# Kernel optimization log

Hardware: AMD Instinct MI355X
Metric: run time of the kernel (lower is better)

The kernel has to match this reference:

```python
import jax, jax.numpy as jnp
import numpy as np

B, N, DH = 256, 32, 128      # batch, n_agents, per-agent hidden
E = 496                       # n_edges (fully connected over 32 agents)
DIM_IN = 2 * DH               # 256, MLP input (concat of two agent states)
DIM_HID = 256
A = 12                        # dim_act
R = 4                         # payoff_rank
DIM_OUT = 2 * R * A           # 96


def setup_inputs() -> dict:
    key = jax.random.key(0)
    ks = jax.random.split(key, 7)
    hidden_states_n = jax.random.normal(ks[0], (B, N, DH), dtype=jnp.float32)
    edges_from = jax.random.randint(ks[1], (E,), 0, N, dtype=jnp.int32).astype(jnp.int64)
    edges_to = jax.random.randint(ks[2], (E,), 0, N, dtype=jnp.int32).astype(jnp.int64)
    # torch.nn.Linear params: W [out, in], b [out]
    W1 = jax.random.normal(ks[3], (DIM_HID, DIM_IN), dtype=jnp.float32) * (1.0 / np.sqrt(DIM_IN))
    b1 = jnp.zeros((DIM_HID,), dtype=jnp.float32)
    W2 = jax.random.normal(ks[4], (DIM_OUT, DIM_HID), dtype=jnp.float32) * (1.0 / np.sqrt(DIM_HID))
    b2 = jnp.zeros((DIM_OUT,), dtype=jnp.float32)
    return {"hidden_states_n": hidden_states_n, "W1": W1, "b1": b1, "W2": W2,
            "b2": b2, "edges_from": edges_from, "edges_to": edges_to}


def reference(hidden_states_n, W1, b1, W2, b2, edges_from, edges_to):
    hf = hidden_states_n[:, edges_from]                     # [B, E, DH]
    ht = hidden_states_n[:, edges_to]                       # [B, E, DH]
    # stack of (from||to, to||from): [2, B, E, 2*DH]
    inp = jnp.stack([jnp.concatenate([hf, ht], axis=-1),
                     jnp.concatenate([ht, hf], axis=-1)], axis=0)
    h = jax.nn.relu(inp @ W1.T + b1)                        # [2, B, E, DIM_HID]
    p = h @ W2.T + b2                                       # [2, B, E, 2*R*A]
    p = p.reshape(2, B, E, R, 2, A)
    # low-rank outer product per rank, summed over ranks: [2, B, E, A, A]
    payoffs = jnp.einsum('sberi,sberj->sbeij', p[..., 0, :], p[..., 1, :])
    # second copy is transposed, then mean over the two directions
    return 0.5 * (payoffs[0] + jnp.swapaxes(payoffs[1], -1, -2))  # [B, E, A, A]
```

## Files before the change

kernel.cpp:

```cpp
#include <hip/hip_runtime.h>

typedef unsigned int uint;
typedef unsigned short ushort_t;
typedef _Float16 f16;

typedef __attribute__((ext_vector_type(8))) _Float16 f16x8;
typedef __attribute__((ext_vector_type(2))) _Float16 f16x2;
typedef __attribute__((ext_vector_type(4))) float f32x4;

#define E_CNT 496

__device__ __forceinline__ uint pack2_f16(float lo, float hi) {
    union { f16x2 h; uint u; } r;
    r.h[0] = (_Float16)lo;
    r.h[1] = (_Float16)hi;
    return r.u;
}

__global__ __launch_bounds__(256) void x_kernel(
    const float* __restrict__ hidden, const float* __restrict__ W1,
    const float* __restrict__ b1, f16* __restrict__ Xout) {
    __shared__ __align__(16) f16 w1s[256 * 128];

    const int tid = threadIdx.x;
    const int half = blockIdx.x & 1;
    const int mblk = blockIdx.x >> 1;

    {
        const int c = tid & 15;
        const int h0 = tid >> 4;
        #pragma unroll
        for (int it = 0; it < 16; ++it) {
            const int h = it * 16 + h0;
            const float* src = W1 + h * 256 + half * 128 + c * 8;
            float4 v0 = *(const float4*)src;
            float4 v1 = *(const float4*)(src + 4);
            uint4 o;
            o.x = pack2_f16(v0.x, v0.y);
            o.y = pack2_f16(v0.z, v0.w);
            o.z = pack2_f16(v1.x, v1.y);
            o.w = pack2_f16(v1.z, v1.w);
            *(uint4*)&w1s[h * 128 + ((c ^ (h & 7)) << 3)] = o;
        }
    }

    const int ln = tid & 63;
    const int waveId = tid >> 6;
    const int quad = ln >> 4;
    const int l16 = ln & 15;
    const int row0 = mblk * 64 + waveId * 16;

    union { uint u[4]; f16x8 v; } af[4];
    const float* arow = hidden + (row0 + l16) * 128 + quad * 8;
    #pragma unroll
    for (int kk = 0; kk < 4; ++kk) {
        float4 v0 = *(const float4*)(arow + kk * 32);
        float4 v1 = *(const float4*)(arow + kk * 32 + 4);
        af[kk].u[0] = pack2_f16(v0.x, v0.y);
        af[kk].u[1] = pack2_f16(v0.z, v0.w);
        af[kk].u[2] = pack2_f16(v1.x, v1.y);
        af[kk].u[3] = pack2_f16(v1.z, v1.w);
    }
    float bh[16];
    #pragma unroll
    for (int nt = 0; nt < 16; ++nt) bh[nt] = 0.5f * b1[nt * 16 + l16];

    __syncthreads();

    f16* xbase = Xout + half * (8192 * 256);
    #pragma unroll 4
    for (int nt = 0; nt < 16; ++nt) {
        const int h = nt * 16 + l16;
        f32x4 acc = (f32x4){0.f, 0.f, 0.f, 0.f};
        #pragma unroll
        for (int kk = 0; kk < 4; ++kk) {
            const int c_log = kk * 4 + quad;
            f16x8 bf = *(const f16x8*)&w1s[h * 128 + ((c_log ^ (h & 7)) << 3)];
            acc = __builtin_amdgcn_mfma_f32_16x16x32_f16(af[kk].v, bf, acc, 0, 0, 0);
        }
        #pragma unroll
        for (int r = 0; r < 4; ++r) {
            const int row = row0 + quad * 4 + r;
            xbase[row * 256 + h] = (_Float16)(acc[r] + bh[nt]);
        }
    }
}

#define PAIR_STRIDE 100
#define R_OFF 800
#define WAVE_PF 1600

__global__ __launch_bounds__(512, 4) void gemm_payoff_kernel(
    const f16* __restrict__ X1, const f16* __restrict__ X2,
    const int* __restrict__ e_f, const int* __restrict__ e_t,
    const float* __restrict__ W2, const float* __restrict__ b2,
    float* __restrict__ out) {

    __shared__ __align__(16) unsigned char smem[51200];
    f16* w2s = (f16*)smem;
    float* pf = (float*)smem;

    const int tid = threadIdx.x;

    #pragma unroll
    for (int j = 0; j < 12; ++j) {
        int idx4 = tid + j * 512;
        int n = idx4 >> 6;
        int k = (idx4 & 63) << 2;
        float4 v = *(const float4*)&W2[n * 256 + k];
        uint2 o;
        o.x = pack2_f16(v.x, v.y);
        o.y = pack2_f16(v.z, v.w);
        *(uint2*)&w2s[n * 264 + k] = o;
    }

    const int ln = tid & 63;
    const int waveId = tid >> 6;
    const int quad = ln >> 4;
    const int l16 = ln & 15;
    const int pl = l16 & 7;
    const int s = l16 >> 3;

    const int bx = blockIdx.x;
    const int lb = (bx & 7) * 124 + (bx >> 3);

    bool f64 = true, t64 = true;
    #pragma unroll
    for (int i = 0; i < 16; ++i) {
        if (e_f[2 * i + 1] != 0) f64 = false;
        if (e_t[2 * i + 1] != 0) t64 = false;
    }

    const int pairBase = lb * 128 + waveId * 16;
    const f16* px1[2];
    const f16* px2[2];
    #pragma unroll
    for (int mt = 0; mt < 2; ++mt) {
        int pair = pairBase + mt * 8 + pl;
        int b = pair / E_CNT;
        int e = pair - b * E_CNT;
        int f = f64 ? e_f[2 * e] : e_f[e];
        int t = t64 ? e_t[2 * e] : e_t[e];
        int n1 = s ? t : f;
        int n2 = s ? f : t;
        px1[mt] = X1 + ((b * 32 + n1) * 256 + quad * 8);
        px2[mt] = X2 + ((b * 32 + n2) * 256 + quad * 8);
    }

    f32x4 acc[2][6];
    #pragma unroll
    for (int mt = 0; mt < 2; ++mt)
        #pragma unroll
        for (int tt = 0; tt < 6; ++tt) acc[mt][tt] = (f32x4){0.f, 0.f, 0.f, 0.f};

    typedef union { uint4 q; f16x8 h; } XU;
    XU G1[2][2], G2[2][2];

    #pragma unroll
    for (int mt = 0; mt < 2; ++mt) {
        G1[0][mt].q = *(const uint4*)(px1[mt] + 0 * 32);
        G2[0][mt].q = *(const uint4*)(px2[mt] + 0 * 32);
        G1[1][mt].q = *(const uint4*)(px1[mt] + 1 * 32);
        G2[1][mt].q = *(const uint4*)(px2[mt] + 1 * 32);
    }

    const f16x8 zero8 = (f16x8){0, 0, 0, 0, 0, 0, 0, 0};

    __syncthreads();

    #pragma unroll
    for (int kk = 0; kk < 8; ++kk) {
        const int buf = kk & 1;
        f16x8 af[2];
        #pragma unroll
        for (int mt = 0; mt < 2; ++mt) {
            f16x8 sum = G1[buf][mt].h + G2[buf][mt].h;
            af[mt] = __builtin_elementwise_max(sum, zero8);
        }
        if (kk < 6) {
            #pragma unroll
            for (int mt = 0; mt < 2; ++mt) {
                G1[buf][mt].q = *(const uint4*)(px1[mt] + (kk + 2) * 32);
                G2[buf][mt].q = *(const uint4*)(px2[mt] + (kk + 2) * 32);
            }
        }
        #pragma unroll
        for (int tt = 0; tt < 6; ++tt) {
            f16x8 bf = *(const f16x8*)&w2s[(tt * 16 + l16) * 264 + kk * 32 + quad * 8];
            acc[0][tt] = __builtin_amdgcn_mfma_f32_16x16x32_f16(af[0], bf, acc[0][tt], 0, 0, 0);
            acc[1][tt] = __builtin_amdgcn_mfma_f32_16x16x32_f16(af[1], bf, acc[1][tt], 0, 0, 0);
        }
    }

    float b2v[6];
    #pragma unroll
    for (int tt = 0; tt < 6; ++tt) b2v[tt] = b2[tt * 16 + l16];

    __syncthreads();

    float* wbase = pf + waveId * WAVE_PF;
    #pragma unroll
    for (int mt = 0; mt < 2; ++mt) {
        #pragma unroll
        for (int tt = 0; tt < 6; ++tt) {
            const int n = tt * 16 + l16;
            const int rr = n / 24;
            const int rem = n - rr * 24;
            const int c01 = (rem >= 12) ? 1 : 0;
            const int a = rem - c01 * 12;
            #pragma unroll
            for (int r = 0; r < 4; ++r) {
                const int row = quad * 4 + r;
                const int s_ = row >> 3;
                const int pl_ = row & 7;
                const int k8 = (s_ ? 4 : 0) + rr;
                const int toL = (c01 == s_) ? 1 : 0;
                wbase[(toL ? 0 : R_OFF) + pl_ * PAIR_STRIDE + a * 8 + k8] = acc[mt][tt][r] + b2v[tt];
            }
        }

        #pragma unroll
        for (int it = 0; it < 2; ++it) {
            int task = it * 64 + ln;
            if (task < 96) {
                int pp = task / 12;
                int i = task - pp * 12;
                const float* Lp = wbase + pp * PAIR_STRIDE + i * 8;
                float4 l0 = *(const float4*)&Lp[0];
                float4 l1 = *(const float4*)&Lp[4];
                float od[12];
                #pragma unroll
                for (int jj = 0; jj < 12; ++jj) {
                    const float* Rp = wbase + R_OFF + pp * PAIR_STRIDE + jj * 8;
                    float4 r0 = *(const float4*)&Rp[0];
                    float4 r1 = *(const float4*)&Rp[4];
                    float d = l0.x * r0.x + l0.y * r0.y + l0.z * r0.z + l0.w * r0.w
                            + l1.x * r1.x + l1.y * r1.y + l1.z * r1.z + l1.w * r1.w;
                    od[jj] = 0.5f * d;
                }
                int outBase = (pairBase + mt * 8 + pp) * 144 + i * 12;
                *(float4*)&out[outBase + 0] = make_float4(od[0], od[1], od[2], od[3]);
                *(float4*)&out[outBase + 4] = make_float4(od[4], od[5], od[6], od[7]);
                *(float4*)&out[outBase + 8] = make_float4(od[8], od[9], od[10], od[11]);
            }
        }
    }
}

extern "C" void kernel_launch(void* const* d_in, const int* in_sizes, int n_in,
                              void* d_out, int out_size, void* d_ws, size_t ws_size,
                              hipStream_t stream) {
    const float* hidden = (const float*)d_in[0];
    const float* W1 = (const float*)d_in[1];
    const float* b1 = (const float*)d_in[2];
    const float* W2 = (const float*)d_in[3];
    const float* b2 = (const float*)d_in[4];
    const int* e_f = (const int*)d_in[5];
    const int* e_t = (const int*)d_in[6];
    float* out = (float*)d_out;

    char* ws = (char*)d_ws;
    f16* X = (f16*)ws;

    x_kernel<<<256, 256, 0, stream>>>(hidden, W1, b1, X);
    gemm_payoff_kernel<<<992, 512, 0, stream>>>(X, X + 8192 * 256, e_f, e_t, W2, b2, out);
}
```

Measured before the change: 137.6 us.

## Restructure X kernel to keep W1 in registers; halve payoff blocks with split W2 staging

The first kernel now keeps each wave's W1 tiles in registers and stages a 64-row tile of hidden states in shared memory instead of staging a full f16 W1 half. It swaps the MFMA operands so each lane writes four packed f16 outputs at once, and it launches twice as many blocks. The payoff kernel drops to 256 threads per block and 26KB of shared memory by staging W2 in two K-halves with extra barriers, which should allow more resident blocks. Scatter offsets are also precomputed. The cost is reloading and converting W2 twice per block and more block-level synchronization.

```diff
diff --git a/kernel.cpp b/kernel.cpp
--- a/kernel.cpp
+++ b/kernel.cpp
@@ -1,7 +1,6 @@
 #include <hip/hip_runtime.h>
 
 typedef unsigned int uint;
-typedef unsigned short ushort_t;
 typedef _Float16 f16;
 
 typedef __attribute__((ext_vector_type(8))) _Float16 f16x8;
@@ -20,68 +19,81 @@
 __global__ __launch_bounds__(256) void x_kernel(
     const float* __restrict__ hidden, const float* __restrict__ W1,
     const float* __restrict__ b1, f16* __restrict__ Xout) {
-    __shared__ __align__(16) f16 w1s[256 * 128];
+    __shared__ __align__(16) float hs[64 * 132];
 
     const int tid = threadIdx.x;
-    const int half = blockIdx.x & 1;
-    const int mblk = blockIdx.x >> 1;
-
-    {
-        const int c = tid & 15;
-        const int h0 = tid >> 4;
-        #pragma unroll
-        for (int it = 0; it < 16; ++it) {
-            const int h = it * 16 + h0;
-            const float* src = W1 + h * 256 + half * 128 + c * 8;
-            float4 v0 = *(const float4*)src;
-            float4 v1 = *(const float4*)(src + 4);
-            uint4 o;
-            o.x = pack2_f16(v0.x, v0.y);
-            o.y = pack2_f16(v0.z, v0.w);
-            o.z = pack2_f16(v1.x, v1.y);
-            o.w = pack2_f16(v1.z, v1.w);
-            *(uint4*)&w1s[h * 128 + ((c ^ (h & 7)) << 3)] = o;
-        }
-    }
-
+    const int rowblock = blockIdx.x >> 2;
+    const int g = blockIdx.x & 3;
     const int ln = tid & 63;
     const int waveId = tid >> 6;
     const int quad = ln >> 4;
     const int l16 = ln & 15;
-    const int row0 = mblk * 64 + waveId * 16;
-
-    union { uint u[4]; f16x8 v; } af[4];
-    const float* arow = hidden + (row0 + l16) * 128 + quad * 8;
-    #pragma unroll
-    for (int kk = 0; kk < 4; ++kk) {
-        float4 v0 = *(const float4*)(arow + kk * 32);
-        float4 v1 = *(const float4*)(arow + kk * 32 + 4);
-        af[kk].u[0] = pack2_f16(v0.x, v0.y);
-        af[kk].u[1] = pack2_f16(v0.z, v0.w);
-        af[kk].u[2] = pack2_f16(v1.x, v1.y);
-        af[kk].u[3] = pack2_f16(v1.z, v1.w);
-    }
-    float bh[16];
-    #pragma unroll
-    for (int nt = 0; nt < 16; ++nt) bh[nt] = 0.5f * b1[nt * 16 + l16];
-
-    __syncthreads();
-
-    f16* xbase = Xout + half * (8192 * 256);
-    #pragma unroll 4
-    for (int nt = 0; nt < 16; ++nt) {
-        const int h = nt * 16 + l16;
-        f32x4 acc = (f32x4){0.f, 0.f, 0.f, 0.f};
+    const int row0 = rowblock * 64;
+
+    union FU { uint u[4]; f16x8 v; };
+    FU wf[2][4];
+    float bh[2][4];
+    #pragma unroll
+    for (int nt = 0; nt < 2; ++nt) {
+        const int t = (g * 4 + waveId) * 2 + nt;
+        const int half = t >> 4;
+        const int htile = t & 15;
+        const float* wrow = W1 + (htile * 16 + l16) * 256 + half * 128 + quad * 8;
         #pragma unroll
         for (int kk = 0; kk < 4; ++kk) {
-            const int c_log = kk * 4 + quad;
-            f16x8 bf = *(const f16x8*)&w1s[h * 128 + ((c_log ^ (h & 7)) << 3)];
-            acc = __builtin_amdgcn_mfma_f32_16x16x32_f16(af[kk].v, bf, acc, 0, 0, 0);
-        }
-        #pragma unroll
-        for (int r = 0; r < 4; ++r) {
-            const int row = row0 + quad * 4 + r;
-            xbase[row * 256 + h] = (_Float16)(acc[r] + bh[nt]);
+            float4 v0 = *(const float4*)(wrow + kk * 32);
+            float4 v1 = *(const float4*)(wrow + kk * 32 + 4);
+            wf[nt][kk].u[0] = pack2_f16(v0.x, v0.y);
+            wf[nt][kk].u[1] = pack2_f16(v0.z, v0.w);
+            wf[nt][kk].u[2] = pack2_f16(v1.x, v1.y);
+            wf[nt][kk].u[3] = pack2_f16(v1.z, v1.w);
+        }
+        #pragma unroll
+        for (int r = 0; r < 4; ++r)
+            bh[nt][r] = 0.5f * b1[htile * 16 + quad * 4 + r];
+    }
+
+    {
+        const float* src = hidden + row0 * 128;
+        #pragma unroll
+        for (int it = 0; it < 8; ++it) {
+            int idx = it * 256 + tid;
+            int r = idx >> 5;
+            int c4 = idx & 31;
+            float4 v = *(const float4*)(src + idx * 4);
+            *(float4*)&hs[r * 132 + c4 * 4] = v;
+        }
+    }
+    __syncthreads();
+
+    #pragma unroll
+    for (int ch = 0; ch < 4; ++ch) {
+        FU hf[4];
+        const float* hrow = &hs[(ch * 16 + l16) * 132 + quad * 8];
+        #pragma unroll
+        for (int kk = 0; kk < 4; ++kk) {
+            float4 v0 = *(const float4*)(hrow + kk * 32);
+            float4 v1 = *(const float4*)(hrow + kk * 32 + 4);
+            hf[kk].u[0] = pack2_f16(v0.x, v0.y);
+            hf[kk].u[1] = pack2_f16(v0.z, v0.w);
+            hf[kk].u[2] = pack2_f16(v1.x, v1.y);
+            hf[kk].u[3] = pack2_f16(v1.z, v1.w);
+        }
+        #pragma unroll
+        for (int nt = 0; nt < 2; ++nt) {
+            const int t = (g * 4 + waveId) * 2 + nt;
+            const int half = t >> 4;
+            const int htile = t & 15;
+            f32x4 acc = (f32x4){0.f, 0.f, 0.f, 0.f};
+            #pragma unroll
+            for (int kk = 0; kk < 4; ++kk)
+                acc = __builtin_amdgcn_mfma_f32_16x16x32_f16(wf[nt][kk].v, hf[kk].v, acc, 0, 0, 0);
+            uint2 o;
+            o.x = pack2_f16(acc[0] + bh[nt][0], acc[1] + bh[nt][1]);
+            o.y = pack2_f16(acc[2] + bh[nt][2], acc[3] + bh[nt][3]);
+            f16* dst = Xout + half * (8192 * 256)
+                     + (row0 + ch * 16 + l16) * 256 + htile * 16 + quad * 4;
+            *(uint2*)dst = o;
         }
     }
 }
@@ -90,30 +102,17 @@
 #define R_OFF 800
 #define WAVE_PF 1600
 
-__global__ __launch_bounds__(512, 4) void gemm_payoff_kernel(
+__global__ __launch_bounds__(256, 4) void gemm_payoff_kernel(
     const f16* __restrict__ X1, const f16* __restrict__ X2,
     const int* __restrict__ e_f, const int* __restrict__ e_t,
     const float* __restrict__ W2, const float* __restrict__ b2,
     float* __restrict__ out) {
 
-    __shared__ __align__(16) unsigned char smem[51200];
+    __shared__ __align__(16) unsigned char smem[26624];
     f16* w2s = (f16*)smem;
     float* pf = (float*)smem;
 
     const int tid = threadIdx.x;
-
-    #pragma unroll
-    for (int j = 0; j < 12; ++j) {
-        int idx4 = tid + j * 512;
-        int n = idx4 >> 6;
-        int k = (idx4 & 63) << 2;
-        float4 v = *(const float4*)&W2[n * 256 + k];
-        uint2 o;
-        o.x = pack2_f16(v.x, v.y);
-        o.y = pack2_f16(v.z, v.w);
-        *(uint2*)&w2s[n * 264 + k] = o;
-    }
-
     const int ln = tid & 63;
     const int waveId = tid >> 6;
     const int quad = ln >> 4;
@@ -122,7 +121,7 @@
     const int s = l16 >> 3;
 
     const int bx = blockIdx.x;
-    const int lb = (bx & 7) * 124 + (bx >> 3);
+    const int lb = (bx & 7) * 248 + (bx >> 3);
 
     bool f64 = true, t64 = true;
     #pragma unroll
@@ -131,7 +130,7 @@
         if (e_t[2 * i + 1] != 0) t64 = false;
     }
 
-    const int pairBase = lb * 128 + waveId * 16;
+    const int pairBase = lb * 64 + waveId * 16;
     const f16* px1[2];
     const f16* px2[2];
     #pragma unroll
@@ -164,12 +163,53 @@
         G2[1][mt].q = *(const uint4*)(px2[mt] + 1 * 32);
     }
 
+    auto stageW2 = [&](int h) {
+        #pragma unroll
+        for (int j = 0; j < 12; ++j) {
+            int idx4 = tid + j * 256;
+            int n = idx4 >> 5;
+            int k4 = idx4 & 31;
+            float4 v = *(const float4*)&W2[n * 256 + h * 128 + k4 * 4];
+            uint2 o;
+            o.x = pack2_f16(v.x, v.y);
+            o.y = pack2_f16(v.z, v.w);
+            *(uint2*)&w2s[n * 136 + k4 * 4] = o;
+        }
+    };
+
     const f16x8 zero8 = (f16x8){0, 0, 0, 0, 0, 0, 0, 0};
 
-    __syncthreads();
-
-    #pragma unroll
-    for (int kk = 0; kk < 8; ++kk) {
+    stageW2(0);
+    __syncthreads();
+
+    #pragma unroll
+    for (int kk = 0; kk < 4; ++kk) {
+        const int buf = kk & 1;
+        f16x8 af[2];
+        #pragma unroll
+        for (int mt = 0; mt < 2; ++mt) {
+            f16x8 sum = G1[buf][mt].h + G2[buf][mt].h;
+            af[mt] = __builtin_elementwise_max(sum, zero8);
+        }
+        #pragma unroll
+        for (int mt = 0; mt < 2; ++mt) {
+            G1[buf][mt].q = *(const uint4*)(px1[mt] + (kk + 2) * 32);
+            G2[buf][mt].q = *(const uint4*)(px2[mt] + (kk + 2) * 32);
+        }
+        #pragma unroll
+        for (int tt = 0; tt < 6; ++tt) {
+            f16x8 bf = *(const f16x8*)&w2s[(tt * 16 + l16) * 136 + kk * 32 + quad * 8];
+            acc[0][tt] = __builtin_amdgcn_mfma_f32_16x16x32_f16(af[0], bf, acc[0][tt], 0, 0, 0);
+            acc[1][tt] = __builtin_amdgcn_mfma_f32_16x16x32_f16(af[1], bf, acc[1][tt], 0, 0, 0);
+        }
+    }
+
+    __syncthreads();
+    stageW2(1);
+    __syncthreads();
+
+    #pragma unroll
+    for (int kk = 4; kk < 8; ++kk) {
         const int buf = kk & 1;
         f16x8 af[2];
         #pragma unroll
@@ -186,7 +226,7 @@
         }
         #pragma unroll
         for (int tt = 0; tt < 6; ++tt) {
-            f16x8 bf = *(const f16x8*)&w2s[(tt * 16 + l16) * 264 + kk * 32 + quad * 8];
+            f16x8 bf = *(const f16x8*)&w2s[(tt * 16 + l16) * 136 + (kk - 4) * 32 + quad * 8];
             acc[0][tt] = __builtin_amdgcn_mfma_f32_16x16x32_f16(af[0], bf, acc[0][tt], 0, 0, 0);
             acc[1][tt] = __builtin_amdgcn_mfma_f32_16x16x32_f16(af[1], bf, acc[1][tt], 0, 0, 0);
         }
@@ -196,6 +236,22 @@
     #pragma unroll
     for (int tt = 0; tt < 6; ++tt) b2v[tt] = b2[tt * 16 + l16];
 
+    int doff[6];
+    {
+        const int s_ = quad >> 1;
+        #pragma unroll
+        for (int tt = 0; tt < 6; ++tt) {
+            int n = tt * 16 + l16;
+            int rr = n / 24;
+            int rem = n - rr * 24;
+            int c01 = (rem >= 12) ? 1 : 0;
+            int a = rem - c01 * 12;
+            int k8 = (s_ ? 4 : 0) + rr;
+            int toL = (c01 == s_) ? 1 : 0;
+            doff[tt] = (toL ? 0 : R_OFF) + (quad & 1) * 4 * PAIR_STRIDE + a * 8 + k8;
+        }
+    }
+
     __syncthreads();
 
     float* wbase = pf + waveId * WAVE_PF;
@@ -203,19 +259,9 @@
     for (int mt = 0; mt < 2; ++mt) {
         #pragma unroll
         for (int tt = 0; tt < 6; ++tt) {
-            const int n = tt * 16 + l16;
-            const int rr = n / 24;
-            const int rem = n - rr * 24;
-            const int c01 = (rem >= 12) ? 1 : 0;
-            const int a = rem - c01 * 12;
             #pragma unroll
             for (int r = 0; r < 4; ++r) {
-                const int row = quad * 4 + r;
-                const int s_ = row >> 3;
-                const int pl_ = row & 7;
-                const int k8 = (s_ ? 4 : 0) + rr;
-                const int toL = (c01 == s_) ? 1 : 0;
-                wbase[(toL ? 0 : R_OFF) + pl_ * PAIR_STRIDE + a * 8 + k8] = acc[mt][tt][r] + b2v[tt];
+                wbase[doff[tt] + r * PAIR_STRIDE] = acc[mt][tt][r] + b2v[tt];
             }
         }
 
@@ -262,6 +308,6 @@
     char* ws = (char*)d_ws;
     f16* X = (f16*)ws;
 
-    x_kernel<<<256, 256, 0, stream>>>(hidden, W1, b1, X);
-    gemm_payoff_kernel<<<992, 512, 0, stream>>>(X, X + 8192 * 256, e_f, e_t, W2, b2, out);
+    x_kernel<<<512, 256, 0, stream>>>(hidden, W1, b1, X);
+    gemm_payoff_kernel<<<1984, 256, 0, stream>>>(X, X + 8192 * 256, e_f, e_t, W2, b2, out);
 }
```

Measured after the change: 144.4 us. +5.0%, slower.
